# Optimization experiments

Measured on AMD Instinct MI355X. Metric: run time of the kernel, lower is better.

Reference implementation:

```python
import jax, jax.numpy as jnp
import numpy as np

HIDDEN = 256
B, L = 4, 4096


def setup_inputs() -> dict:
    key = jax.random.key(0)
    k_in, k_q, k_k, k_v, k_len = jax.random.split(key, 5)
    inputs = jax.random.normal(k_in, (B, L, HIDDEN), dtype=jnp.float32)
    # torch.rand -> uniform [0,1)
    W_query = jax.random.uniform(k_q, (HIDDEN, HIDDEN), dtype=jnp.float32)
    W_key = jax.random.uniform(k_k, (HIDDEN, HIDDEN), dtype=jnp.float32)
    W_value = jax.random.uniform(k_v, (HIDDEN, HIDDEN), dtype=jnp.float32)
    lengths = jax.random.randint(k_len, (B,), 1, L + 1, dtype=jnp.int64)
    return {"inputs": inputs, "W_query": W_query, "W_key": W_key,
            "W_value": W_value, "lengths": lengths}


def reference(inputs, W_query, W_key, W_value, lengths):
    # lengths is unused by the original module (no masking applied).
    # QKV projections (batched matmul with shared weight)
    queries = jnp.einsum('blh,hd->bld', inputs, W_query)
    keys = jnp.einsum('blh,hd->bld', inputs, W_key)
    values = jnp.einsum('blh,hd->bld', inputs, W_value)
    # scaled dot-product attention, full [B, L, L] scores as in original
    scale = 1.0 / jnp.sqrt(jnp.asarray(HIDDEN, dtype=inputs.dtype))
    attn_scores = jnp.einsum('bqd,bkd->bqk', queries, keys) * scale
    attentions = jax.nn.softmax(attn_scores, axis=-1)
    weighted = jnp.einsum('bqk,bkd->bqd', attentions, values)
    return weighted
```

## Files before the change

### kernel.cpp

```cpp
#include <hip/hip_runtime.h>


typedef __bf16 bf16x8 __attribute__((ext_vector_type(8)));
typedef _Float16 f16x8 __attribute__((ext_vector_type(8)));
typedef _Float16 f16x4 __attribute__((ext_vector_type(4)));
typedef float floatx4 __attribute__((ext_vector_type(4)));

#define MFMA16B(a, b, c) __builtin_amdgcn_mfma_f32_16x16x32_bf16(a, b, c, 0, 0, 0)
#define MFMA16F(a, b, c) __builtin_amdgcn_mfma_f32_16x16x32_f16(a, b, c, 0, 0, 0)
#define GLOAD_LDS16(g, l)                                                  \
  __builtin_amdgcn_global_load_lds(                                        \
      (const __attribute__((address_space(1))) void *)(g),                 \
      (__attribute__((address_space(3))) void *)(l), 16, 0, 0)

#define HID 256
#define LSEQ 4096
#define NB 4
#define NTOK (NB * LSEQ)
#define PLANE ((size_t)NTOK * HID)
#define NSPLIT 4
#define QSCALE 0.09016844005556021f


__device__ __forceinline__ void split_bf16(float v, __bf16 &h, __bf16 &l) {
  h = (__bf16)v;
  l = (__bf16)(v - (float)h);
}

template <int N>
__device__ __forceinline__ float dpp_ror(float v) {
  return __builtin_bit_cast(float,
      __builtin_amdgcn_update_dpp(0, __builtin_bit_cast(int, v),
                                  0x120 + N, 0xf, 0xf, true));
}
__device__ __forceinline__ float row_sum16(float v) {
  v += dpp_ror<1>(v);
  v += dpp_ror<2>(v);
  v += dpp_ror<4>(v);
  v += dpp_ror<8>(v);
  return v;
}
__device__ __forceinline__ float row_max16(float v) {
  v = fmaxf(v, dpp_ror<1>(v));
  v = fmaxf(v, dpp_ror<2>(v));
  v = fmaxf(v, dpp_ror<4>(v));
  v = fmaxf(v, dpp_ror<8>(v));
  return v;
}

__global__ __launch_bounds__(256) void wsplit(const float *__restrict__ Wq,
                                              const float *__restrict__ Wk,
                                              const float *__restrict__ Wv,
                                              __bf16 *__restrict__ Wht,
                                              __bf16 *__restrict__ Wlt) {
  __shared__ float tile[32][256];
  const int wsel = blockIdx.x;
  const int hb = blockIdx.y;
  const float *W = (wsel == 0) ? Wq : (wsel == 1) ? Wk : Wv;
  __bf16 *oh = Wht + wsel * HID * HID;
  __bf16 *ol = Wlt + wsel * HID * HID;
  const int t = threadIdx.x;
  #pragma unroll
  for (int p = 0; p < 8; ++p) {
    int r = p * 4 + (t >> 6);
    int c = (t & 63) * 4;
    *(floatx4 *)&tile[r][c] = *(const floatx4 *)&W[(hb * 32 + r) * HID + c];
  }
  __syncthreads();
  #pragma unroll
  for (int q = 0; q < 4; ++q) {
    int n = q * 64 + (t >> 2);
    int hs = (t & 3) * 8;
    bf16x8 hh, ll;
    #pragma unroll
    for (int i = 0; i < 8; ++i) {
      float v = tile[hs + i][n];
      __bf16 h, l;
      split_bf16(v, h, l);
      hh[i] = h; ll[i] = l;
    }
    *(bf16x8 *)&oh[n * HID + hb * 32 + hs] = hh;
    *(bf16x8 *)&ol[n * HID + hb * 32 + hs] = ll;
  }
}

__global__ __launch_bounds__(256, 2) void qkv_proj(const float *__restrict__ X,
                                                   const __bf16 *__restrict__ Wht,
                                                   const __bf16 *__restrict__ Wlt,
                                                   _Float16 *__restrict__ Qf,
                                                   _Float16 *__restrict__ Kf,
                                                   _Float16 *__restrict__ Vf) {
  __shared__ __bf16 WhS[64 * 256];
  __shared__ __bf16 WlS[64 * 256];
  _Float16 *Tf = (_Float16 *)WhS;

  const int mtile = blockIdx.x;
  const int col0 = blockIdx.y * 64;
  const int tid = threadIdx.x;
  const int w4 = tid >> 6;
  const int lane = tid & 63;
  const int quad = lane >> 4;
  const int ln = lane & 15;
  const int arow = mtile * 64 + w4 * 16 + ln;

  bf16x8 ah[8], al[8];
  #pragma unroll
  for (int kc = 0; kc < 8; ++kc) {
    const float *xp = X + (size_t)arow * HID + kc * 32 + quad * 8;
    floatx4 x0 = *(const floatx4 *)xp;
    floatx4 x1 = *(const floatx4 *)(xp + 4);
    #pragma unroll
    for (int j = 0; j < 4; ++j) {
      __bf16 h, l;
      split_bf16(x0[j], h, l); ah[kc][j] = h; al[kc][j] = l;
      split_bf16(x1[j], h, l); ah[kc][4 + j] = h; al[kc][4 + j] = l;
    }
  }

  const int srow = tid >> 2;
  const int sseg = tid & 3;

  bf16x8 pwh[8], pwl[8];
  {
    const size_t wbase = (size_t)(col0 + srow) * HID;
    #pragma unroll
    for (int j = 0; j < 8; ++j) {
      const int chunk = j * 4 + sseg;
      pwh[j] = *(const bf16x8 *)&Wht[wbase + chunk * 8];
      pwl[j] = *(const bf16x8 *)&Wlt[wbase + chunk * 8];
    }
  }

  for (int w = 0; w < 3; ++w) {
    __syncthreads();
    #pragma unroll
    for (int j = 0; j < 8; ++j) {
      const int chunk = j * 4 + sseg;
      const int dst = srow * 256 + ((chunk ^ (srow & 7)) << 3);
      *(bf16x8 *)&WhS[dst] = pwh[j];
      *(bf16x8 *)&WlS[dst] = pwl[j];
    }
    __syncthreads();

    if (w < 2) {
      const size_t wbase = (size_t)(w + 1) * HID * HID + (size_t)(col0 + srow) * HID;
      #pragma unroll
      for (int j = 0; j < 8; ++j) {
        const int chunk = j * 4 + sseg;
        pwh[j] = *(const bf16x8 *)&Wht[wbase + chunk * 8];
        pwl[j] = *(const bf16x8 *)&Wlt[wbase + chunk * 8];
      }
    }

    floatx4 acc[4] = {};
    #pragma unroll
    for (int kc = 0; kc < 8; ++kc) {
      #pragma unroll
      for (int nt = 0; nt < 4; ++nt) {
        const int a = (nt * 16 + ln) * 256 + (((kc * 4 + quad) ^ (ln & 7)) << 3);
        bf16x8 bh = *(const bf16x8 *)&WhS[a];
        bf16x8 bl = *(const bf16x8 *)&WlS[a];
        acc[nt] = MFMA16B(ah[kc], bh, acc[nt]);
        acc[nt] = MFMA16B(ah[kc], bl, acc[nt]);
        acc[nt] = MFMA16B(al[kc], bh, acc[nt]);
      }
    }

    if (w == 0) {
      #pragma unroll
      for (int nt = 0; nt < 4; ++nt) {
        #pragma unroll
        for (int r = 0; r < 4; ++r) {
          const int orow = mtile * 64 + w4 * 16 + quad * 4 + r;
          const int ocol = col0 + nt * 16 + ln;
          Qf[(size_t)orow * HID + ocol] = (_Float16)(acc[nt][r] * QSCALE);
        }
      }
    } else if (w == 1) {
      __syncthreads();
      #pragma unroll
      for (int nt = 0; nt < 4; ++nt) {
        #pragma unroll
        for (int r = 0; r < 4; ++r) {
          const int tok_l = w4 * 16 + quad * 4 + r;
          const int h_l = nt * 16 + ln;
          Tf[tok_l * 72 + h_l] = (_Float16)acc[nt][r];
        }
      }
      __syncthreads();
      #pragma unroll
      for (int i = 0; i < 2; ++i) {
        const int c = i * 256 + tid;
        const int lane_f = c & 63;
        const int ntf = (c >> 6) & 1;
        const int kcL = (c >> 7) & 1;
        const int t2 = (c >> 8) & 1;
        const int qf = lane_f >> 4;
        const int lnf = lane_f & 15;
        const int tok_l = t2 * 32 + ntf * 16 + lnf;
        f16x8 v = *(const f16x8 *)&Tf[tok_l * 72 + kcL * 32 + qf * 8];
        const int T = mtile * 2 + t2;
        const int kc = (col0 >> 5) + kcL;
        *(f16x8 *)&Kf[(size_t)T * 8192 + ((ntf * 8 + kc) * 64 + lane_f) * 8] = v;
      }
    } else {
      __syncthreads();
      #pragma unroll
      for (int nt = 0; nt < 4; ++nt) {
        #pragma unroll
        for (int r = 0; r < 4; ++r) {
          const int tok_l = w4 * 16 + quad * 4 + r;
          const int d_l = nt * 16 + ln;
          Tf[d_l * 72 + tok_l] = (_Float16)acc[nt][r];
        }
      }
      __syncthreads();
      #pragma unroll
      for (int i = 0; i < 2; ++i) {
        const int c = i * 256 + tid;
        const int lane_f = c & 63;
        const int dtL = (c >> 6) & 3;
        const int t2 = (c >> 8) & 1;
        const int qf = lane_f >> 4;
        const int lnf = lane_f & 15;
        const int d_l = dtL * 16 + lnf;
        f16x8 v = *(const f16x8 *)&Tf[d_l * 72 + t2 * 32 + qf * 8];
        const int T = mtile * 2 + t2;
        const int dt = (col0 >> 4) + dtL;
        *(f16x8 *)&Vf[(size_t)(T * 16 + dt) * 512 + lane_f * 8] = v;
      }
    }
  }
}

__global__ __launch_bounds__(256, 2) void attn(const _Float16 *__restrict__ Qf,
                                               const _Float16 *__restrict__ Kf,
                                               const _Float16 *__restrict__ Vf,
                                               _Float16 *__restrict__ Op,
                                               float *__restrict__ Mp,
                                               float *__restrict__ Lp) {
  __shared__ _Float16 KS[2][8192];
  __shared__ _Float16 VS[2][8192];
  __shared__ _Float16 PsS[4 * 16 * 40];

  const int bx = blockIdx.x;
  const int ks = bx & 3;
  const int qt = bx >> 2;
  const int b = qt >> 6;
  const int qtl = qt & 63;
  const int tid = threadIdx.x;
  const int w4 = tid >> 6;
  const int lane = tid & 63;
  const int quad = lane >> 4;
  const int ln = lane & 15;
  const int T0 = b * 128 + ks * 32;

  const int qtok = b * LSEQ + qtl * 64 + w4 * 16 + ln;
  f16x8 q[8];
  #pragma unroll
  for (int kc = 0; kc < 8; ++kc)
    q[kc] = *(const f16x8 *)&Qf[(size_t)qtok * HID + kc * 32 + quad * 8];

  const _Float16 *kuni = Kf + (size_t)T0 * 8192;
  const _Float16 *vuni = Vf + (size_t)T0 * 8192;
  const int koff = tid * 8;
  const int voff = lane * 8;

  #pragma unroll
  for (int i = 0; i < 4; ++i)
    GLOAD_LDS16(kuni + i * 2048 + koff, &KS[0][i * 2048 + koff]);
  #pragma unroll
  for (int i = 0; i < 4; ++i)
    GLOAD_LDS16(vuni + i * 2048 + koff, &VS[0][i * 2048 + koff]);
  #pragma unroll
  for (int i = 0; i < 4; ++i)
    GLOAD_LDS16(kuni + 8192 + i * 2048 + koff, &KS[1][i * 2048 + koff]);
  #pragma unroll
  for (int i = 0; i < 4; ++i)
    GLOAD_LDS16(vuni + 8192 + i * 2048 + koff, &VS[1][i * 2048 + koff]);

  float m[4] = {-1e30f, -1e30f, -1e30f, -1e30f};
  float l[4] = {0.f, 0.f, 0.f, 0.f};
  floatx4 o[16] = {};
  _Float16 *ps = PsS + w4 * (16 * 40);

#define ATTN_TILE(TT, BUF, WAITN, DOISSUE)                                   \
  {                                                                          \
    asm volatile("s_waitcnt vmcnt(" #WAITN ")" ::: "memory");                \
    __builtin_amdgcn_s_barrier();                                            \
    __builtin_amdgcn_sched_barrier(0);                                       \
    const _Float16 *Kb = KS[BUF];                                            \
    const _Float16 *Vb = VS[BUF];                                            \
    floatx4 s0, s1;                                                          \
    {                                                                        \
      floatx4 pa0 = {}, pb0 = {}, pa1 = {}, pb1 = {};                        \
      __builtin_amdgcn_s_setprio(1);                                         \
      _Pragma("unroll")                                                      \
      for (int kc = 0; kc < 4; ++kc) {                                       \
        pa0 = MFMA16F(q[kc], *(const f16x8 *)(Kb + kc * 512 + voff), pa0);   \
        pb0 = MFMA16F(q[4 + kc], *(const f16x8 *)(Kb + (4 + kc) * 512 + voff), pb0); \
        pa1 = MFMA16F(q[kc], *(const f16x8 *)(Kb + (8 + kc) * 512 + voff), pa1);     \
        pb1 = MFMA16F(q[4 + kc], *(const f16x8 *)(Kb + (12 + kc) * 512 + voff), pb1);\
      }                                                                      \
      __builtin_amdgcn_s_setprio(0);                                         \
      s0 = pa0 + pb0;                                                        \
      s1 = pa1 + pb1;                                                        \
    }                                                                        \
    float alpha[4];                                                          \
    _Pragma("unroll")                                                        \
    for (int r = 0; r < 4; ++r) {                                            \
      const float tmax = row_max16(fmaxf(s0[r], s1[r]));                     \
      const float mn = fmaxf(m[r], tmax);                                    \
      const float al = exp2f(m[r] - mn);                                     \
      const float p0 = exp2f(s0[r] - mn);                                    \
      const float p1 = exp2f(s1[r] - mn);                                    \
      s0[r] = p0; s1[r] = p1;                                                \
      l[r] = l[r] * al + row_sum16(p0 + p1);                                 \
      m[r] = mn;                                                             \
      alpha[r] = al;                                                         \
    }                                                                        \
    _Pragma("unroll")                                                        \
    for (int r = 0; r < 4; ++r) {                                            \
      ps[(quad * 4 + r) * 40 + ln] = (_Float16)s0[r];                        \
      ps[(quad * 4 + r) * 40 + 16 + ln] = (_Float16)s1[r];                   \
    }                                                                        \
    const float amin =                                                       \
        fminf(fminf(alpha[0], alpha[1]), fminf(alpha[2], alpha[3]));         \
    if (__any(amin < 1.0f)) {                                                \
      _Pragma("unroll")                                                      \
      for (int dt = 0; dt < 16; ++dt) {                                      \
        o[dt][0] *= alpha[0]; o[dt][1] *= alpha[1];                          \
        o[dt][2] *= alpha[2]; o[dt][3] *= alpha[3];                          \
      }                                                                      \
    }                                                                        \
    const f16x8 paf = *(const f16x8 *)&ps[ln * 40 + quad * 8];               \
    __builtin_amdgcn_s_setprio(1);                                           \
    _Pragma("unroll")                                                        \
    for (int dt = 0; dt < 16; ++dt)                                          \
      o[dt] = MFMA16F(paf, *(const f16x8 *)(Vb + dt * 512 + voff), o[dt]);   \
    __builtin_amdgcn_s_setprio(0);                                           \
    __builtin_amdgcn_sched_barrier(0);                                       \
    __builtin_amdgcn_s_barrier();                                            \
    __builtin_amdgcn_sched_barrier(0);                                       \
    if (DOISSUE) {                                                           \
      const _Float16 *ksrc = kuni + (size_t)(TT + 2) * 8192 + koff;          \
      const _Float16 *vsrc = vuni + (size_t)(TT + 2) * 8192 + koff;          \
      _Pragma("unroll")                                                      \
      for (int i = 0; i < 4; ++i)                                            \
        GLOAD_LDS16(ksrc + i * 2048, &KS[BUF][i * 2048 + koff]);             \
      _Pragma("unroll")                                                      \
      for (int i = 0; i < 4; ++i)                                            \
        GLOAD_LDS16(vsrc + i * 2048, &VS[BUF][i * 2048 + koff]);             \
    }                                                                        \
  }

  for (int jm = 0; jm < 15; ++jm) {
    const int t0 = 2 * jm;
    ATTN_TILE(t0, 0, 8, 1)
    ATTN_TILE(t0 + 1, 1, 8, 1)
  }
  ATTN_TILE(30, 0, 8, 0)
  ATTN_TILE(31, 1, 0, 0)
#undef ATTN_TILE

  const int rowbase = b * LSEQ + qtl * 64 + w4 * 16 + quad * 4;
  #pragma unroll
  for (int dt = 0; dt < 16; ++dt)
    #pragma unroll
    for (int r = 0; r < 4; ++r)
      Op[(size_t)ks * PLANE + (size_t)(rowbase + r) * HID + dt * 16 + ln] =
          (_Float16)o[dt][r];
  if (ln == 0) {
    #pragma unroll
    for (int r = 0; r < 4; ++r) {
      Mp[ks * NTOK + rowbase + r] = m[r];
      Lp[ks * NTOK + rowbase + r] = l[r];
    }
  }
}

__global__ __launch_bounds__(256) void merge(const _Float16 *__restrict__ Op,
                                             const float *__restrict__ Mp,
                                             const float *__restrict__ Lp,
                                             float *__restrict__ Out) {
  const int row = blockIdx.x * 4 + (threadIdx.x >> 6);
  const int c = (threadIdx.x & 63) * 4;
  float ms[NSPLIT], ls[NSPLIT];
  #pragma unroll
  for (int s = 0; s < NSPLIT; ++s) {
    ms[s] = Mp[s * NTOK + row];
    ls[s] = Lp[s * NTOK + row];
  }
  const float M = fmaxf(fmaxf(ms[0], ms[1]), fmaxf(ms[2], ms[3]));
  float e[NSPLIT], den = 0.f;
  #pragma unroll
  for (int s = 0; s < NSPLIT; ++s) {
    e[s] = exp2f(ms[s] - M);
    den += ls[s] * e[s];
  }
  const float inv = 1.0f / den;
  floatx4 out = {};
  #pragma unroll
  for (int s = 0; s < NSPLIT; ++s) {
    const f16x4 a = *(const f16x4 *)&Op[(size_t)s * PLANE + (size_t)row * HID + c];
    const float w = e[s] * inv;
    #pragma unroll
    for (int i = 0; i < 4; ++i) out[i] += w * (float)a[i];
  }
  *(floatx4 *)&Out[(size_t)row * HID + c] = out;
}

extern "C" void kernel_launch(void *const *d_in, const int *in_sizes, int n_in,
                              void *d_out, int out_size, void *d_ws, size_t ws_size,
                              hipStream_t stream) {
  const float *X = (const float *)d_in[0];
  const float *Wq = (const float *)d_in[1];
  const float *Wk = (const float *)d_in[2];
  const float *Wv = (const float *)d_in[3];

  _Float16 *ws = (_Float16 *)d_ws;
  _Float16 *Qf = ws;
  _Float16 *Kf = Qf + PLANE;
  _Float16 *Vf = Kf + PLANE;
  __bf16 *Wht = (__bf16 *)(Vf + PLANE);
  __bf16 *Wlt = Wht + 3 * HID * HID;
  _Float16 *Op = (_Float16 *)(Wlt + 3 * HID * HID);
  float *Mp = (float *)(Op + NSPLIT * PLANE);
  float *Lp = Mp + NSPLIT * NTOK;

  wsplit<<<dim3(3, 8), 256, 0, stream>>>(Wq, Wk, Wv, Wht, Wlt);
  qkv_proj<<<dim3(256, 4), 256, 0, stream>>>(X, Wht, Wlt, Qf, Kf, Vf);
  attn<<<NTOK / 64 * NSPLIT, 256, 0, stream>>>(Qf, Kf, Vf, Op, Mp, Lp);
  merge<<<NTOK / 4, 256, 0, stream>>>(Op, Mp, Lp, (float *)d_out);
}
```

Baseline: 226.7 us.

## Compute transposed scores so P stays in registers, drop LDS round-trip

Swaps the MFMA operand order so the score tile comes out transposed, with each lane holding one query's scores. Softmax row max and sum then reduce over a few shuffles instead of DPP row reductions, and the probability fragment is packed straight into registers for the PV MFMA, removing the per-tile LDS store and load of P. The V layout writer is permuted to match. The pipeline is also cut from two tiles in flight to a single prefetch with a full vmcnt(0) wait each iteration, which may expose more load latency.

```diff
diff --git a/kernel.cpp b/kernel.cpp
--- a/kernel.cpp
+++ b/kernel.cpp
@@ -25,27 +25,6 @@
 __device__ __forceinline__ void split_bf16(float v, __bf16 &h, __bf16 &l) {
   h = (__bf16)v;
   l = (__bf16)(v - (float)h);
-}
-
-template <int N>
-__device__ __forceinline__ float dpp_ror(float v) {
-  return __builtin_bit_cast(float,
-      __builtin_amdgcn_update_dpp(0, __builtin_bit_cast(int, v),
-                                  0x120 + N, 0xf, 0xf, true));
-}
-__device__ __forceinline__ float row_sum16(float v) {
-  v += dpp_ror<1>(v);
-  v += dpp_ror<2>(v);
-  v += dpp_ror<4>(v);
-  v += dpp_ror<8>(v);
-  return v;
-}
-__device__ __forceinline__ float row_max16(float v) {
-  v = fmaxf(v, dpp_ror<1>(v));
-  v = fmaxf(v, dpp_ror<2>(v));
-  v = fmaxf(v, dpp_ror<4>(v));
-  v = fmaxf(v, dpp_ror<8>(v));
-  return v;
 }
 
 __global__ __launch_bounds__(256) void wsplit(const float *__restrict__ Wq,
@@ -224,7 +203,11 @@
         const int qf = lane_f >> 4;
         const int lnf = lane_f & 15;
         const int d_l = dtL * 16 + lnf;
-        f16x8 v = *(const f16x8 *)&Tf[d_l * 72 + t2 * 32 + qf * 8];
+        f16x4 lo = *(const f16x4 *)&Tf[d_l * 72 + t2 * 32 + 4 * qf];
+        f16x4 hi = *(const f16x4 *)&Tf[d_l * 72 + t2 * 32 + 16 + 4 * qf];
+        f16x8 v;
+        v[0] = lo[0]; v[1] = lo[1]; v[2] = lo[2]; v[3] = lo[3];
+        v[4] = hi[0]; v[5] = hi[1]; v[6] = hi[2]; v[7] = hi[3];
         const int T = mtile * 2 + t2;
         const int dt = (col0 >> 4) + dtL;
         *(f16x8 *)&Vf[(size_t)(T * 16 + dt) * 512 + lane_f * 8] = v;
@@ -241,7 +224,6 @@
                                                float *__restrict__ Lp) {
   __shared__ _Float16 KS[2][8192];
   __shared__ _Float16 VS[2][8192];
-  __shared__ _Float16 PsS[4 * 16 * 40];
 
   const int bx = blockIdx.x;
   const int ks = bx & 3;
@@ -272,110 +254,94 @@
   #pragma unroll
   for (int i = 0; i < 4; ++i)
     GLOAD_LDS16(vuni + i * 2048 + koff, &VS[0][i * 2048 + koff]);
-  #pragma unroll
-  for (int i = 0; i < 4; ++i)
-    GLOAD_LDS16(kuni + 8192 + i * 2048 + koff, &KS[1][i * 2048 + koff]);
-  #pragma unroll
-  for (int i = 0; i < 4; ++i)
-    GLOAD_LDS16(vuni + 8192 + i * 2048 + koff, &VS[1][i * 2048 + koff]);
-
-  float m[4] = {-1e30f, -1e30f, -1e30f, -1e30f};
-  float l[4] = {0.f, 0.f, 0.f, 0.f};
+
+  float m = -1e30f;
+  float l = 0.f;
   floatx4 o[16] = {};
-  _Float16 *ps = PsS + w4 * (16 * 40);
-
-#define ATTN_TILE(TT, BUF, WAITN, DOISSUE)                                   \
-  {                                                                          \
-    asm volatile("s_waitcnt vmcnt(" #WAITN ")" ::: "memory");                \
-    __builtin_amdgcn_s_barrier();                                            \
-    __builtin_amdgcn_sched_barrier(0);                                       \
-    const _Float16 *Kb = KS[BUF];                                            \
-    const _Float16 *Vb = VS[BUF];                                            \
-    floatx4 s0, s1;                                                          \
-    {                                                                        \
-      floatx4 pa0 = {}, pb0 = {}, pa1 = {}, pb1 = {};                        \
-      __builtin_amdgcn_s_setprio(1);                                         \
-      _Pragma("unroll")                                                      \
-      for (int kc = 0; kc < 4; ++kc) {                                       \
-        pa0 = MFMA16F(q[kc], *(const f16x8 *)(Kb + kc * 512 + voff), pa0);   \
-        pb0 = MFMA16F(q[4 + kc], *(const f16x8 *)(Kb + (4 + kc) * 512 + voff), pb0); \
-        pa1 = MFMA16F(q[kc], *(const f16x8 *)(Kb + (8 + kc) * 512 + voff), pa1);     \
-        pb1 = MFMA16F(q[4 + kc], *(const f16x8 *)(Kb + (12 + kc) * 512 + voff), pb1);\
-      }                                                                      \
-      __builtin_amdgcn_s_setprio(0);                                         \
-      s0 = pa0 + pb0;                                                        \
-      s1 = pa1 + pb1;                                                        \
-    }                                                                        \
-    float alpha[4];                                                          \
-    _Pragma("unroll")                                                        \
-    for (int r = 0; r < 4; ++r) {                                            \
-      const float tmax = row_max16(fmaxf(s0[r], s1[r]));                     \
-      const float mn = fmaxf(m[r], tmax);                                    \
-      const float al = exp2f(m[r] - mn);                                     \
-      const float p0 = exp2f(s0[r] - mn);                                    \
-      const float p1 = exp2f(s1[r] - mn);                                    \
-      s0[r] = p0; s1[r] = p1;                                                \
-      l[r] = l[r] * al + row_sum16(p0 + p1);                                 \
-      m[r] = mn;                                                             \
-      alpha[r] = al;                                                         \
-    }                                                                        \
-    _Pragma("unroll")                                                        \
-    for (int r = 0; r < 4; ++r) {                                            \
-      ps[(quad * 4 + r) * 40 + ln] = (_Float16)s0[r];                        \
-      ps[(quad * 4 + r) * 40 + 16 + ln] = (_Float16)s1[r];                   \
-    }                                                                        \
-    const float amin =                                                       \
-        fminf(fminf(alpha[0], alpha[1]), fminf(alpha[2], alpha[3]));         \
-    if (__any(amin < 1.0f)) {                                                \
-      _Pragma("unroll")                                                      \
-      for (int dt = 0; dt < 16; ++dt) {                                      \
-        o[dt][0] *= alpha[0]; o[dt][1] *= alpha[1];                          \
-        o[dt][2] *= alpha[2]; o[dt][3] *= alpha[3];                          \
-      }                                                                      \
-    }                                                                        \
-    const f16x8 paf = *(const f16x8 *)&ps[ln * 40 + quad * 8];               \
-    __builtin_amdgcn_s_setprio(1);                                           \
-    _Pragma("unroll")                                                        \
-    for (int dt = 0; dt < 16; ++dt)                                          \
-      o[dt] = MFMA16F(paf, *(const f16x8 *)(Vb + dt * 512 + voff), o[dt]);   \
-    __builtin_amdgcn_s_setprio(0);                                           \
-    __builtin_amdgcn_sched_barrier(0);                                       \
-    __builtin_amdgcn_s_barrier();                                            \
-    __builtin_amdgcn_sched_barrier(0);                                       \
-    if (DOISSUE) {                                                           \
-      const _Float16 *ksrc = kuni + (size_t)(TT + 2) * 8192 + koff;          \
-      const _Float16 *vsrc = vuni + (size_t)(TT + 2) * 8192 + koff;          \
-      _Pragma("unroll")                                                      \
-      for (int i = 0; i < 4; ++i)                                            \
-        GLOAD_LDS16(ksrc + i * 2048, &KS[BUF][i * 2048 + koff]);             \
-      _Pragma("unroll")                                                      \
-      for (int i = 0; i < 4; ++i)                                            \
-        GLOAD_LDS16(vsrc + i * 2048, &VS[BUF][i * 2048 + koff]);             \
-    }                                                                        \
-  }
-
-  for (int jm = 0; jm < 15; ++jm) {
-    const int t0 = 2 * jm;
-    ATTN_TILE(t0, 0, 8, 1)
-    ATTN_TILE(t0 + 1, 1, 8, 1)
-  }
-  ATTN_TILE(30, 0, 8, 0)
-  ATTN_TILE(31, 1, 0, 0)
-#undef ATTN_TILE
-
-  const int rowbase = b * LSEQ + qtl * 64 + w4 * 16 + quad * 4;
-  #pragma unroll
-  for (int dt = 0; dt < 16; ++dt)
-    #pragma unroll
-    for (int r = 0; r < 4; ++r)
-      Op[(size_t)ks * PLANE + (size_t)(rowbase + r) * HID + dt * 16 + ln] =
-          (_Float16)o[dt][r];
-  if (ln == 0) {
-    #pragma unroll
-    for (int r = 0; r < 4; ++r) {
-      Mp[ks * NTOK + rowbase + r] = m[r];
-      Lp[ks * NTOK + rowbase + r] = l[r];
-    }
+
+  for (int t = 0; t < 32; ++t) {
+    const int buf = t & 1;
+    asm volatile("s_waitcnt vmcnt(0)" ::: "memory");
+    __builtin_amdgcn_s_barrier();
+    __builtin_amdgcn_sched_barrier(0);
+    if (t < 31) {
+      const _Float16 *ksrc = kuni + (size_t)(t + 1) * 8192 + koff;
+      const _Float16 *vsrc = vuni + (size_t)(t + 1) * 8192 + koff;
+      #pragma unroll
+      for (int i = 0; i < 4; ++i)
+        GLOAD_LDS16(ksrc + i * 2048, &KS[buf ^ 1][i * 2048 + koff]);
+      #pragma unroll
+      for (int i = 0; i < 4; ++i)
+        GLOAD_LDS16(vsrc + i * 2048, &VS[buf ^ 1][i * 2048 + koff]);
+    }
+    const _Float16 *Kb = KS[buf];
+    const _Float16 *Vb = VS[buf];
+
+    floatx4 s0, s1;
+    {
+      floatx4 pa0 = {}, pb0 = {}, pa1 = {}, pb1 = {};
+      __builtin_amdgcn_s_setprio(1);
+      #pragma unroll
+      for (int kc = 0; kc < 4; ++kc) {
+        pa0 = MFMA16F(*(const f16x8 *)(Kb + kc * 512 + voff), q[kc], pa0);
+        pb0 = MFMA16F(*(const f16x8 *)(Kb + (4 + kc) * 512 + voff), q[4 + kc], pb0);
+        pa1 = MFMA16F(*(const f16x8 *)(Kb + (8 + kc) * 512 + voff), q[kc], pa1);
+        pb1 = MFMA16F(*(const f16x8 *)(Kb + (12 + kc) * 512 + voff), q[4 + kc], pb1);
+      }
+      __builtin_amdgcn_s_setprio(0);
+      s0 = pa0 + pb0;
+      s1 = pa1 + pb1;
+    }
+
+    float tmax = fmaxf(fmaxf(fmaxf(s0[0], s0[1]), fmaxf(s0[2], s0[3])),
+                       fmaxf(fmaxf(s1[0], s1[1]), fmaxf(s1[2], s1[3])));
+    tmax = fmaxf(tmax, __shfl_xor(tmax, 16));
+    tmax = fmaxf(tmax, __shfl_xor(tmax, 32));
+    const float mn = fmaxf(m, tmax);
+    const float al = exp2f(m - mn);
+    #pragma unroll
+    for (int i = 0; i < 4; ++i) {
+      s0[i] = exp2f(s0[i] - mn);
+      s1[i] = exp2f(s1[i] - mn);
+    }
+    float rs = ((s0[0] + s0[1]) + (s0[2] + s0[3])) +
+               ((s1[0] + s1[1]) + (s1[2] + s1[3]));
+    rs += __shfl_xor(rs, 16);
+    rs += __shfl_xor(rs, 32);
+    l = l * al + rs;
+    m = mn;
+
+    f16x8 pf;
+    pf[0] = (_Float16)s0[0]; pf[1] = (_Float16)s0[1];
+    pf[2] = (_Float16)s0[2]; pf[3] = (_Float16)s0[3];
+    pf[4] = (_Float16)s1[0]; pf[5] = (_Float16)s1[1];
+    pf[6] = (_Float16)s1[2]; pf[7] = (_Float16)s1[3];
+
+    if (__any(al < 1.0f)) {
+      #pragma unroll
+      for (int dt = 0; dt < 16; ++dt) {
+        o[dt][0] *= al; o[dt][1] *= al; o[dt][2] *= al; o[dt][3] *= al;
+      }
+    }
+
+    __builtin_amdgcn_s_setprio(1);
+    #pragma unroll
+    for (int dt = 0; dt < 16; ++dt)
+      o[dt] = MFMA16F(*(const f16x8 *)(Vb + dt * 512 + voff), pf, o[dt]);
+    __builtin_amdgcn_s_setprio(0);
+    __builtin_amdgcn_sched_barrier(0);
+  }
+
+  #pragma unroll
+  for (int dt = 0; dt < 16; ++dt) {
+    f16x4 v4;
+    v4[0] = (_Float16)o[dt][0]; v4[1] = (_Float16)o[dt][1];
+    v4[2] = (_Float16)o[dt][2]; v4[3] = (_Float16)o[dt][3];
+    *(f16x4 *)&Op[(size_t)ks * PLANE + (size_t)qtok * HID + dt * 16 + quad * 4] = v4;
+  }
+  if (quad == 0) {
+    Mp[ks * NTOK + qtok] = m;
+    Lp[ks * NTOK + qtok] = l;
   }
 }
 
```

Result: no change. 222.4 us (-1.9%).
